# Optimization experiments

Measured on AMD Instinct MI355X. Metric: run time of the kernel, lower is better.

## Reference

```python
import jax, jax.numpy as jnp
import numpy as np

K = 2          # top-k experts
LN_EPS = 1e-5  # torch LayerNorm default


def setup_inputs() -> dict:
    key = jax.random.key(0)
    ks = jax.random.split(key, 8)
    B, D, E, H, O = 16384, 512, 16, 128, 512
    s = 0.02
    return {
        "x": jax.random.normal(ks[0], (B, D), dtype=jnp.float32),
        "gate_W": jax.random.normal(ks[1], (D, E), dtype=jnp.float32) * s,
        "gate_b": jnp.zeros((E,), dtype=jnp.float32),
        "W1": jax.random.normal(ks[2], (E, D, H), dtype=jnp.float32) * s,
        "b1": jnp.zeros((E, H), dtype=jnp.float32),
        "ln_g": jnp.ones((E, H), dtype=jnp.float32),
        "ln_b": jnp.zeros((E, H), dtype=jnp.float32),
        "W2": jax.random.normal(ks[3], (E, H, O), dtype=jnp.float32) * s,
        "b2": jnp.zeros((E, O), dtype=jnp.float32),
    }


def reference(x, gate_W, gate_b, W1, b1, ln_g, ln_b, W2, b2):
    B = x.shape[0]
    E = gate_W.shape[1]

    # gating
    gate_scores = x @ gate_W + gate_b                       # [B, E]
    topk_val, topk_idx = jax.lax.top_k(gate_scores, K)      # [B, K]

    # load-balancing aux loss
    mask = jnp.zeros((B, E), x.dtype).at[jnp.arange(B)[:, None], topk_idx].set(1.0)
    expert_usage = mask.mean(axis=0)                        # [E]
    load_balance = jnp.mean((expert_usage - 1.0 / E) ** 2)
    logp = jax.nn.log_softmax(gate_scores, axis=-1)
    entropy = (-(jnp.exp(logp) * logp).sum(axis=-1)).mean()
    aux_loss = load_balance - 0.1 * entropy

    gate_weights = jax.nn.softmax(topk_val, axis=-1)        # [B, K]

    # dense all-expert compute (as in the original torch.stack over experts)
    h = jnp.einsum('bd,edh->beh', x, W1) + b1               # [B, E, H]
    h = jax.nn.gelu(h, approximate=False)                   # torch default exact GELU
    mu = h.mean(axis=-1, keepdims=True)
    var = ((h - mu) ** 2).mean(axis=-1, keepdims=True)
    h = (h - mu) * jax.lax.rsqrt(var + LN_EPS) * ln_g + ln_b
    expert_out = jnp.einsum('beh,eho->beo', h, W2) + b2     # [B, E, O]

    # gather top-k expert outputs and combine
    sel = jnp.take_along_axis(expert_out, topk_idx[:, :, None], axis=1)  # [B, K, O]
    out = (sel * gate_weights[:, :, None]).sum(axis=1)      # [B, O]
    return out, aux_loss
```

## Files before the change

### kernel.cpp

```cpp
#include <hip/hip_runtime.h>

#define BROWS 16384
#define DDIM  512
#define NEXP  16
#define HDIM  128
#define ODIM  512
#define MAXTILES 528

typedef __attribute__((ext_vector_type(8))) short bf16x8;
typedef __attribute__((ext_vector_type(4))) float f32x4;

typedef const __attribute__((address_space(1))) unsigned GA;
typedef __attribute__((address_space(3))) unsigned LA;
#define GLD16(g, l) __builtin_amdgcn_global_load_lds((GA*)(g), (LA*)(l), 16, 0, 0)

static __device__ __forceinline__ unsigned short f2bf(float f) {
    union { float f; unsigned u; } v; v.f = f;
    unsigned r = v.u + 0x7fffu + ((v.u >> 16) & 1u);
    return (unsigned short)(r >> 16);
}
static __device__ __forceinline__ float bf2f(unsigned short h) {
    union { unsigned u; float f; } v; v.u = ((unsigned)h) << 16;
    return v.f;
}

__global__ __launch_bounds__(256)
void prep0_kernel(const float* __restrict__ gW, float* __restrict__ gwT,
                  int* __restrict__ cnt, float* __restrict__ ent_acc) {
    const int b = blockIdx.x, tid = threadIdx.x;
    if (b == 32) {
        if (tid < 16) cnt[tid] = 0;
        if (tid == 16) ent_acc[0] = 0.f;
        return;
    }
    int i = b * 256 + tid;
    int d = i >> 4, e = i & 15;
    gwT[e * 512 + d] = gW[i];
}

__global__ __launch_bounds__(256)
void gate_kernel(const float* __restrict__ x, const float* __restrict__ gwTg,
                 const float* __restrict__ gb,
                 int* cnt, float* ent_acc, int* bucket, int* topk_e, float* topk_w,
                 unsigned short* __restrict__ xb,
                 const float* __restrict__ W1, unsigned short* __restrict__ w1b,
                 const float* __restrict__ W2, unsigned short* __restrict__ w2t) {
    __shared__ __align__(16) char sbuf[33792];
    __shared__ int lcnt[16];
    __shared__ int gbase[16];
    __shared__ int entpack[32];
    __shared__ float entf;

    const int b = blockIdx.x;
    const int tid = threadIdx.x;

    if (b >= 1024) {
        if (b < 1536) {
            float (*tile)[33] = (float(*)[33])sbuf;
            int bb = b - 1024;
            int e = bb >> 5;
            int rem = bb & 31;
            int ks = rem >> 2;
            int cb = (rem & 3) * 32;
            const float* src = W1 + ((size_t)e * 512 + ks * 64) * 128 + cb;
            int c = tid & 31, r8 = tid >> 5;
            #pragma unroll
            for (int p = 0; p < 8; ++p)
                tile[p * 8 + r8][c] = src[(size_t)(p * 8 + r8) * 128 + c];
            __syncthreads();
            int k = tid & 63, c4 = tid >> 6;
            unsigned short* dst = w1b + (((size_t)e * 8 + ks) * 128 + cb) * 64;
            #pragma unroll
            for (int p = 0; p < 8; ++p)
                dst[(size_t)(c4 + p * 4) * 64 + k] = f2bf(tile[k][c4 + p * 4]);
        } else {
            float (*tile)[33] = (float(*)[33])sbuf;
            int bb = b - 1536;
            int e = bb >> 6;
            int rem = bb & 63;
            int r0 = (rem >> 4) * 32;
            int c0 = (rem & 15) * 32;
            const float* in = W2 + (size_t)e * HDIM * ODIM;
            unsigned short* out = w2t + (size_t)e * HDIM * ODIM;
            int tx = tid & 31, ty = tid >> 5;
            for (int i = ty; i < 32; i += 8)
                tile[i][tx] = in[(size_t)(r0 + i) * ODIM + c0 + tx];
            __syncthreads();
            for (int i = ty; i < 32; i += 8)
                out[(size_t)(c0 + i) * HDIM + r0 + tx] = f2bf(tile[tx][i]);
        }
        return;
    }

    float (*xs)[4][132] = (float(*)[4][132])sbuf;
    const int rb = b * 16;

    #pragma unroll
    for (int k = 0; k < 8; ++k) {
        int idx = tid + k * 256;
        int row = idx >> 7, c4 = idx & 127;
        float4 v = *reinterpret_cast<const float4*>(x + (size_t)(rb + row) * DDIM + c4 * 4);
        int dq = c4 >> 5, j = c4 & 31;
        *reinterpret_cast<float4*>(&xs[row][dq][j * 4]) = v;
        uint2 p;
        p.x = (unsigned)f2bf(v.x) | ((unsigned)f2bf(v.y) << 16);
        p.y = (unsigned)f2bf(v.z) | ((unsigned)f2bf(v.w) << 16);
        *reinterpret_cast<uint2*>(xb + (size_t)(rb + row) * DDIM + c4 * 4) = p;
    }
    if (tid < 16) lcnt[tid] = 0;
    if (tid == 0) entf = 0.f;

    const int wave = tid >> 6, lane = tid & 63;
    const int e = lane & 15, dq = lane >> 4;
    const int r0 = wave * 4;

    const float4* gw4 = reinterpret_cast<const float4*>(gwTg) + e * 128 + dq * 32;
    float gbe = gb[e];
    __syncthreads();

    float a0 = 0.f, a1 = 0.f, a2 = 0.f, a3 = 0.f;
    #pragma unroll
    for (int j = 0; j < 32; ++j) {
        float4 g  = gw4[j];
        float4 v0 = *reinterpret_cast<const float4*>(&xs[r0 + 0][dq][j * 4]);
        float4 v1 = *reinterpret_cast<const float4*>(&xs[r0 + 1][dq][j * 4]);
        float4 v2 = *reinterpret_cast<const float4*>(&xs[r0 + 2][dq][j * 4]);
        float4 v3 = *reinterpret_cast<const float4*>(&xs[r0 + 3][dq][j * 4]);
        a0 = fmaf(v0.x, g.x, a0); a0 = fmaf(v0.y, g.y, a0); a0 = fmaf(v0.z, g.z, a0); a0 = fmaf(v0.w, g.w, a0);
        a1 = fmaf(v1.x, g.x, a1); a1 = fmaf(v1.y, g.y, a1); a1 = fmaf(v1.z, g.z, a1); a1 = fmaf(v1.w, g.w, a1);
        a2 = fmaf(v2.x, g.x, a2); a2 = fmaf(v2.y, g.y, a2); a2 = fmaf(v2.z, g.z, a2); a2 = fmaf(v2.w, g.w, a2);
        a3 = fmaf(v3.x, g.x, a3); a3 = fmaf(v3.y, g.y, a3); a3 = fmaf(v3.z, g.z, a3); a3 = fmaf(v3.w, g.w, a3);
    }
    a0 += __shfl_xor(a0, 16); a0 += __shfl_xor(a0, 32);
    a1 += __shfl_xor(a1, 16); a1 += __shfl_xor(a1, 32);
    a2 += __shfl_xor(a2, 16); a2 += __shfl_xor(a2, 32);
    a3 += __shfl_xor(a3, 16); a3 += __shfl_xor(a3, 32);

    float sc = (dq == 0) ? a0 : (dq == 1) ? a1 : (dq == 2) ? a2 : a3;
    sc += gbe;

    float v0 = sc, v1 = -1e30f;
    int   i0 = e,  i1 = 255;
    #pragma unroll
    for (int k = 1; k <= 8; k <<= 1) {
        float o0 = __shfl_xor(v0, k), o1 = __shfl_xor(v1, k);
        int   oi0 = __shfl_xor(i0, k), oi1 = __shfl_xor(i1, k);
        bool gt = (o0 > v0) || (o0 == v0 && oi0 < i0);
        float n0 = gt ? o0 : v0;  int ni0 = gt ? oi0 : i0;
        float c  = gt ? v0 : o0;  int ci  = gt ? i0 : oi0;
        float d  = gt ? o1 : v1;  int di_ = gt ? oi1 : i1;
        bool g2 = (c > d) || (c == d && ci < di_);
        v0 = n0; i0 = ni0;
        v1 = g2 ? c : d;  i1 = g2 ? ci : di_;
    }

    float t = sc - v0;
    float ex = expf(t);
    float Z = ex, S1 = ex * t;
    #pragma unroll
    for (int k = 1; k <= 8; k <<= 1) {
        Z  += __shfl_xor(Z, k);
        S1 += __shfl_xor(S1, k);
    }
    float entloc = logf(Z) - S1 / Z;
    float w0 = 1.0f / (1.0f + expf(v1 - v0));

    if (e == 0) {
        int row = rb + r0 + dq;
        topk_e[row * 2]     = i0;
        topk_e[row * 2 + 1] = i1;
        topk_w[row * 2]     = w0;
        topk_w[row * 2 + 1] = 1.0f - w0;
        int ib = r0 + dq;
        int lp0 = atomicAdd(&lcnt[i0], 1);
        entpack[ib * 2]     = (row << 1) | (i0 << 15) | (lp0 << 19);
        int lp1 = atomicAdd(&lcnt[i1], 1);
        entpack[ib * 2 + 1] = ((row << 1) | 1) | (i1 << 15) | (lp1 << 19);
        atomicAdd(&entf, entloc);
    }
    __syncthreads();
    if (tid < 16) gbase[tid] = atomicAdd(&cnt[tid], lcnt[tid]);
    if (tid == 0) atomicAdd(ent_acc, entf);
    __syncthreads();
    if (tid < 32) {
        int p = entpack[tid];
        int rowslot = p & 0x7FFF;
        int ee = (p >> 15) & 15;
        int lpos = p >> 19;
        bucket[ee * BROWS + gbase[ee] + lpos] = rowslot;
    }
}

__global__ __launch_bounds__(256, 2)
void ffn_kernel(const unsigned short* __restrict__ xb,
                const unsigned short* __restrict__ w1b,
                const unsigned short* __restrict__ w2t,
                const float* __restrict__ b1, const float* __restrict__ ln_g,
                const float* __restrict__ ln_b, const float* __restrict__ topk_w,
                const int* __restrict__ cnt, const int* __restrict__ bucket,
                const float* __restrict__ ent_acc, float* __restrict__ outp,
                unsigned short* __restrict__ contrib) {
    const int b = blockIdx.x;
    const int tid = threadIdx.x;

    int e = -1, t = 0;
    {
        int o = 0;
        #pragma unroll
        for (int k = 0; k < 16; ++k) {
            int nt = (cnt[k] + 63) >> 6;
            if (b >= o && b < o + nt) { e = k; t = b - o; }
            o += nt;
        }
    }
    if (e < 0) {
        if (b == MAXTILES - 1 && tid == 0) {
            float lb = 0.f;
            for (int k = 0; k < 16; ++k) {
                float u = (float)cnt[k] * (1.f / 16384.f) - 0.0625f;
                lb += u * u;
            }
            lb *= (1.f / 16.f);
            outp[0] = lb - 0.1f * (ent_acc[0] * (1.f / 16384.f));
        }
        return;
    }
    int n = cnt[e];
    int base = t * 64;
    int rows = n - base; if (rows > 64) rows = 64;

    __shared__ __align__(16) char smem[51712];

    const int wave = tid >> 6, lane = tid & 63;
    const int l15 = lane & 15, l4 = lane >> 4;
    const int bbase = e * BROWS + base;

    if (tid < 64) {
        int idx = tid < rows ? tid : (rows - 1);
        int rs = bucket[bbase + idx];
        *(int*)(smem + 51200 + tid * 4) = rs;
        *(float*)(smem + 51456 + tid * 4) = topk_w[rs];
    }

    const int lsw = (((lane & 7) ^ ((lane >> 3) & 7)) << 4);
    int ar0 = wave * 16 + (lane >> 3);
    int ar1 = ar0 + 8;
    size_t grow0 = (size_t)(bucket[bbase + (ar0 < rows ? ar0 : rows - 1)] >> 1) * 1024;
    size_t grow1 = (size_t)(bucket[bbase + (ar1 < rows ? ar1 : rows - 1)] >> 1) * 1024;
    const char* xbp = (const char*)xb;
    const char* w1e = (const char*)w1b + (size_t)e * 131072;
    const char* w2e = (const char*)w2t + (size_t)e * 131072;
    const int sw2e = (((lane & 15) ^ (lane >> 4)) << 4);
    const int sw2o = sw2e ^ 64;

#define STAGE1(ks_, buf_) do { \
    char* ab_ = smem + (buf_) * 8192; \
    char* bb_ = smem + 16384 + (buf_) * 16384; \
    GLD16(xbp + grow0 + (ks_) * 128 + lsw, ab_ + (wave * 2 + 0) * 1024); \
    GLD16(xbp + grow1 + (ks_) * 128 + lsw, ab_ + (wave * 2 + 1) * 1024); \
    const char* s1_ = w1e + (ks_) * 16384 + ((lane >> 3) << 7) + lsw; \
    GLD16(s1_ + (wave * 4 + 0) * 1024, bb_ + (wave * 4 + 0) * 1024); \
    GLD16(s1_ + (wave * 4 + 1) * 1024, bb_ + (wave * 4 + 1) * 1024); \
    GLD16(s1_ + (wave * 4 + 2) * 1024, bb_ + (wave * 4 + 2) * 1024); \
    GLD16(s1_ + (wave * 4 + 3) * 1024, bb_ + (wave * 4 + 3) * 1024); \
} while (0)

#define STAGE2(ns_, buf_) do { \
    char* bb_ = smem + 16384 + (buf_) * 16384; \
    const char* s2_ = w2e + (size_t)(ns_) * 16384 + ((lane >> 4) << 8); \
    GLD16(s2_ + (wave * 4 + 0) * 1024 + sw2e, bb_ + (wave * 4 + 0) * 1024); \
    GLD16(s2_ + (wave * 4 + 1) * 1024 + sw2o, bb_ + (wave * 4 + 1) * 1024); \
    GLD16(s2_ + (wave * 4 + 2) * 1024 + sw2e, bb_ + (wave * 4 + 2) * 1024); \
    GLD16(s2_ + (wave * 4 + 3) * 1024 + sw2o, bb_ + (wave * 4 + 3) * 1024); \
} while (0)

    STAGE1(0, 0);
    f32x4 acc1[4][2];
    #pragma unroll
    for (int r = 0; r < 4; ++r)
        #pragma unroll
        for (int c = 0; c < 2; ++c)
            acc1[r][c] = (f32x4){0.f, 0.f, 0.f, 0.f};

    #pragma unroll
    for (int ks = 0; ks < 8; ++ks) {
        const int cur = ks & 1;
        if (ks < 7) {
            STAGE1(ks + 1, cur ^ 1);
            asm volatile("s_waitcnt vmcnt(6)" ::: "memory");
        } else {
            asm volatile("s_waitcnt vmcnt(0)" ::: "memory");
        }
        asm volatile("s_barrier" ::: "memory");
        const char* ab = smem + cur * 8192;
        const char* bb = smem + 16384 + cur * 16384;
        #pragma unroll
        for (int ks2 = 0; ks2 < 2; ++ks2) {
            const int cb = (((ks2 * 4 + l4) ^ (l15 & 7)) << 4);
            bf16x8 a[4], bg[2];
            #pragma unroll
            for (int r = 0; r < 4; ++r)
                a[r] = *(const bf16x8*)(ab + (r * 16 + l15) * 128 + cb);
            bg[0] = *(const bf16x8*)(bb + (wave * 32 + l15) * 128 + cb);
            bg[1] = *(const bf16x8*)(bb + (wave * 32 + 16 + l15) * 128 + cb);
            #pragma unroll
            for (int r = 0; r < 4; ++r) {
                acc1[r][0] = __builtin_amdgcn_mfma_f32_16x16x32_bf16(a[r], bg[0], acc1[r][0], 0, 0, 0);
                acc1[r][1] = __builtin_amdgcn_mfma_f32_16x16x32_bf16(a[r], bg[1], acc1[r][1], 0, 0, 0);
            }
        }
        asm volatile("s_waitcnt lgkmcnt(0)\n\ts_barrier" ::: "memory");
    }

    STAGE2(0, 0);

    const float* b1e = b1 + e * HDIM;
    const int c0 = wave * 32 + l15, c1 = c0 + 16;
    float bias0 = b1e[c0], bias1 = b1e[c1];
    #pragma unroll
    for (int r = 0; r < 4; ++r)
        #pragma unroll
        for (int i = 0; i < 4; ++i) {
            int row = r * 16 + l4 * 4 + i;
            float v0 = acc1[r][0][i] + bias0;
            float v1 = acc1[r][1][i] + bias1;
            v0 = 0.5f * v0 * (1.0f + erff(v0 * 0.70710678f));
            v1 = 0.5f * v1 * (1.0f + erff(v1 * 0.70710678f));
            acc1[r][0][i] = v0; acc1[r][1][i] = v1;
            float s = v0 + v1, ss = v0 * v0 + v1 * v1;
            s  += __shfl_xor(s, 1);  s  += __shfl_xor(s, 2);
            s  += __shfl_xor(s, 4);  s  += __shfl_xor(s, 8);
            ss += __shfl_xor(ss, 1); ss += __shfl_xor(ss, 2);
            ss += __shfl_xor(ss, 4); ss += __shfl_xor(ss, 8);
            if (l15 == 0) {
                *(float*)(smem + 49152 + row * 32 + wave * 8)     = s;
                *(float*)(smem + 49152 + row * 32 + wave * 8 + 4) = ss;
            }
        }
    asm volatile("s_waitcnt lgkmcnt(0)\n\ts_barrier" ::: "memory");

    {
        const float* lge = ln_g + e * HDIM;
        const float* lbe = ln_b + e * HDIM;
        float g0 = lge[c0], g1 = lge[c1], be0 = lbe[c0], be1 = lbe[c1];
        #pragma unroll
        for (int r = 0; r < 4; ++r)
            #pragma unroll
            for (int i = 0; i < 4; ++i) {
                int row = r * 16 + l4 * 4 + i;
                float4 p0 = *(const float4*)(smem + 49152 + row * 32);
                float4 p1 = *(const float4*)(smem + 49152 + row * 32 + 16);
                float s  = p0.x + p0.z + p1.x + p1.z;
                float ss = p0.y + p0.w + p1.y + p1.w;
                float mean = s * 0.0078125f;
                float var  = fmaf(-mean, mean, ss * 0.0078125f);
                float rstd = rsqrtf(var + 1e-5f);
                float w = *(const float*)(smem + 51456 + row * 4);
                float h0 = ((acc1[r][0][i] - mean) * rstd * g0 + be0) * w;
                float h1 = ((acc1[r][1][i] - mean) * rstd * g1 + be1) * w;
                int wr = (row & 7) << 4;
                *(unsigned short*)(smem + row * 256 + ((c0 * 2) ^ wr)) = f2bf(h0);
                *(unsigned short*)(smem + row * 256 + ((c1 * 2) ^ wr)) = f2bf(h1);
            }
    }
    asm volatile("s_waitcnt lgkmcnt(0)\n\ts_barrier" ::: "memory");

    bf16x8 A2[4][4];
    #pragma unroll
    for (int r = 0; r < 4; ++r)
        #pragma unroll
        for (int kk = 0; kk < 4; ++kk)
            A2[r][kk] = *(const bf16x8*)(smem + (r * 16 + l15) * 256 + ((((kk * 4 + l4) ^ (l15 & 7))) << 4));
    asm volatile("s_waitcnt lgkmcnt(0)\n\ts_barrier" ::: "memory");

    STAGE2(1, 1);
    char* patch = smem + wave * 3072;
    const int rsoff = (*(const int*)(smem + 51200 + lane * 4)) << 10;
    char* cw = (char*)contrib + rsoff + wave * 32;

    #pragma unroll
    for (int ns = 0; ns < 8; ++ns) {
        if (ns < 7) {
            asm volatile("s_waitcnt lgkmcnt(0)" ::: "memory");
            if (ns > 0) STAGE2(ns + 1, (ns + 1) & 1);
        }
        if (ns == 0)      asm volatile("s_waitcnt vmcnt(4)" ::: "memory");
        else if (ns < 7)  asm volatile("s_waitcnt vmcnt(6)" ::: "memory");
        else              asm volatile("s_waitcnt vmcnt(2)" ::: "memory");

        const char* bb = smem + 16384 + (ns & 1) * 16384;
        bf16x8 Bf[4];
        #pragma unroll
        for (int kk = 0; kk < 4; ++kk)
            Bf[kk] = *(const bf16x8*)(bb + (wave * 16 + l15) * 256 + ((((kk * 4 + l4) ^ (l15 & 7))) << 4));

        f32x4 acc2[4];
        #pragma unroll
        for (int r = 0; r < 4; ++r) acc2[r] = (f32x4){0.f, 0.f, 0.f, 0.f};
        #pragma unroll
        for (int kk = 0; kk < 4; ++kk)
            #pragma unroll
            for (int r = 0; r < 4; ++r)
                acc2[r] = __builtin_amdgcn_mfma_f32_16x16x32_bf16(A2[r][kk], Bf[kk], acc2[r], 0, 0, 0);

        #pragma unroll
        for (int r = 0; r < 4; ++r)
            #pragma unroll
            for (int i = 0; i < 4; ++i)
                *(unsigned short*)(patch + (r * 16 + l4 * 4 + i) * 48 + l15 * 2) = f2bf(acc2[r][i]);
        bf16x8 p0 = *(const bf16x8*)(patch + lane * 48);
        bf16x8 p1 = *(const bf16x8*)(patch + lane * 48 + 16);
        *(bf16x8*)(cw + ns * 128)      = p0;
        *(bf16x8*)(cw + ns * 128 + 16) = p1;
    }
#undef STAGE1
#undef STAGE2
}

__global__ __launch_bounds__(256)
void combine_kernel(const unsigned short* __restrict__ contrib, const int* __restrict__ topk_e,
                    const float* __restrict__ topk_w, const float* __restrict__ b2,
                    float* __restrict__ out) {
    int idx = blockIdx.x * 256 + threadIdx.x;
    int row = idx >> 6;
    int cb = (idx & 63) << 3;
    int e0 = topk_e[row * 2], e1 = topk_e[row * 2 + 1];
    float w0 = topk_w[row * 2], w1 = topk_w[row * 2 + 1];
    bf16x8 c0 = *reinterpret_cast<const bf16x8*>(contrib + (size_t)row * 1024 + cb);
    bf16x8 c1 = *reinterpret_cast<const bf16x8*>(contrib + (size_t)row * 1024 + 512 + cb);
    const float* b20 = b2 + e0 * ODIM + cb;
    const float* b21 = b2 + e1 * ODIM + cb;
    float res[8];
    #pragma unroll
    for (int j = 0; j < 8; ++j)
        res[j] = bf2f((unsigned short)c0[j]) + bf2f((unsigned short)c1[j]) + w0 * b20[j] + w1 * b21[j];
    float4 o0 = {res[0], res[1], res[2], res[3]};
    float4 o1 = {res[4], res[5], res[6], res[7]};
    *reinterpret_cast<float4*>(out + (size_t)row * ODIM + cb) = o0;
    *reinterpret_cast<float4*>(out + (size_t)row * ODIM + cb + 4) = o1;
}

extern "C" void kernel_launch(void* const* d_in, const int* in_sizes, int n_in,
                              void* d_out, int out_size, void* d_ws, size_t ws_size,
                              hipStream_t stream) {
    const float* x    = (const float*)d_in[0];
    const float* gW   = (const float*)d_in[1];
    const float* gb   = (const float*)d_in[2];
    const float* W1   = (const float*)d_in[3];
    const float* b1   = (const float*)d_in[4];
    const float* ln_g = (const float*)d_in[5];
    const float* ln_b = (const float*)d_in[6];
    const float* W2   = (const float*)d_in[7];
    const float* b2   = (const float*)d_in[8];
    float* out = (float*)d_out;

    char* ws = (char*)d_ws;
    int*   cnt      = (int*)(ws);
    float* ent_acc  = (float*)(ws + 64);
    int*   topk_e   = (int*)(ws + 4096);
    float* topk_w   = (float*)(ws + 135168);
    int*   bucket   = (int*)(ws + 266240);
    unsigned short* xb      = (unsigned short*)(ws + 1314816);
    unsigned short* w1b     = (unsigned short*)(ws + 18092032);
    unsigned short* w2t     = (unsigned short*)(ws + 20189184);
    unsigned short* contrib = (unsigned short*)(ws + 22286336);
    float* gwT = (float*)(ws + 22286336);

    prep0_kernel<<<33, 256, 0, stream>>>(gW, gwT, cnt, ent_acc);
    gate_kernel<<<2560, 256, 0, stream>>>(x, gwT, gb, cnt, ent_acc, bucket, topk_e, topk_w, xb,
                                          W1, w1b, W2, w2t);
    ffn_kernel<<<MAXTILES, 256, 0, stream>>>(xb, w1b, w2t, b1, ln_g, ln_b, topk_w, cnt, bucket,
                                             ent_acc, out + (out_size - 1), contrib);
    combine_kernel<<<(BROWS * ODIM / 8) / 256, 256, 0, stream>>>(contrib, topk_e, topk_w, b2, out);
}
```

Measured before the change: 86.87 us.

## Fuse top-k combine into FFN epilogue via atomic adds into zeroed output

Removes the separate combine kernel and the bf16 contrib buffer. The prep kernel now zeroes the output, and the FFN kernel adds each expert's gate-weighted result plus bias directly into the output rows with float atomicAdd. This avoids writing and re-reading the intermediate buffer. In exchange it issues one scalar atomic per output element, with scattered row addresses, and the summation order of the two experts is no longer fixed.

```diff
diff --git a/kernel.cpp b/kernel.cpp
--- a/kernel.cpp
+++ b/kernel.cpp
@@ -19,23 +19,26 @@
     unsigned r = v.u + 0x7fffu + ((v.u >> 16) & 1u);
     return (unsigned short)(r >> 16);
 }
-static __device__ __forceinline__ float bf2f(unsigned short h) {
-    union { unsigned u; float f; } v; v.u = ((unsigned)h) << 16;
-    return v.f;
-}
 
 __global__ __launch_bounds__(256)
 void prep0_kernel(const float* __restrict__ gW, float* __restrict__ gwT,
-                  int* __restrict__ cnt, float* __restrict__ ent_acc) {
+                  int* __restrict__ cnt, float* __restrict__ ent_acc,
+                  float* __restrict__ out) {
     const int b = blockIdx.x, tid = threadIdx.x;
-    if (b == 32) {
+    if (b < 32) {
+        int i = b * 256 + tid;
+        int d = i >> 4, e = i & 15;
+        gwT[e * 512 + d] = gW[i];
+    } else if (b == 32) {
         if (tid < 16) cnt[tid] = 0;
         if (tid == 16) ent_acc[0] = 0.f;
-        return;
-    }
-    int i = b * 256 + tid;
-    int d = i >> 4, e = i & 15;
-    gwT[e * 512 + d] = gW[i];
+    } else {
+        float4* o4 = reinterpret_cast<float4*>(out);
+        int i0 = (b - 33) * 256 + tid;
+        #pragma unroll
+        for (int k = 0; k < 4; ++k)
+            o4[i0 + k * 524288] = (float4){0.f, 0.f, 0.f, 0.f};
+    }
 }
 
 __global__ __launch_bounds__(256)
@@ -198,8 +201,8 @@
                 const float* __restrict__ b1, const float* __restrict__ ln_g,
                 const float* __restrict__ ln_b, const float* __restrict__ topk_w,
                 const int* __restrict__ cnt, const int* __restrict__ bucket,
-                const float* __restrict__ ent_acc, float* __restrict__ outp,
-                unsigned short* __restrict__ contrib) {
+                const float* __restrict__ ent_acc, const float* __restrict__ b2,
+                float* __restrict__ out, float* __restrict__ outp) {
     const int b = blockIdx.x;
     const int tid = threadIdx.x;
 
@@ -374,9 +377,7 @@
     asm volatile("s_waitcnt lgkmcnt(0)\n\ts_barrier" ::: "memory");
 
     STAGE2(1, 1);
-    char* patch = smem + wave * 3072;
-    const int rsoff = (*(const int*)(smem + 51200 + lane * 4)) << 10;
-    char* cw = (char*)contrib + rsoff + wave * 32;
+    const float* b2e = b2 + e * ODIM;
 
     #pragma unroll
     for (int ns = 0; ns < 8; ++ns) {
@@ -403,41 +404,22 @@
             for (int r = 0; r < 4; ++r)
                 acc2[r] = __builtin_amdgcn_mfma_f32_16x16x32_bf16(A2[r][kk], Bf[kk], acc2[r], 0, 0, 0);
 
+        const int col = ns * 64 + wave * 16 + l15;
+        const float b2v = b2e[col];
         #pragma unroll
         for (int r = 0; r < 4; ++r)
             #pragma unroll
-            for (int i = 0; i < 4; ++i)
-                *(unsigned short*)(patch + (r * 16 + l4 * 4 + i) * 48 + l15 * 2) = f2bf(acc2[r][i]);
-        bf16x8 p0 = *(const bf16x8*)(patch + lane * 48);
-        bf16x8 p1 = *(const bf16x8*)(patch + lane * 48 + 16);
-        *(bf16x8*)(cw + ns * 128)      = p0;
-        *(bf16x8*)(cw + ns * 128 + 16) = p1;
+            for (int i = 0; i < 4; ++i) {
+                int row = r * 16 + l4 * 4 + i;
+                if (row < rows) {
+                    int rs = *(const int*)(smem + 51200 + row * 4);
+                    float wv = *(const float*)(smem + 51456 + row * 4);
+                    atomicAdd(out + (size_t)(rs >> 1) * ODIM + col, acc2[r][i] + wv * b2v);
+                }
+            }
     }
 #undef STAGE1
 #undef STAGE2
-}
-
-__global__ __launch_bounds__(256)
-void combine_kernel(const unsigned short* __restrict__ contrib, const int* __restrict__ topk_e,
-                    const float* __restrict__ topk_w, const float* __restrict__ b2,
-                    float* __restrict__ out) {
-    int idx = blockIdx.x * 256 + threadIdx.x;
-    int row = idx >> 6;
-    int cb = (idx & 63) << 3;
-    int e0 = topk_e[row * 2], e1 = topk_e[row * 2 + 1];
-    float w0 = topk_w[row * 2], w1 = topk_w[row * 2 + 1];
-    bf16x8 c0 = *reinterpret_cast<const bf16x8*>(contrib + (size_t)row * 1024 + cb);
-    bf16x8 c1 = *reinterpret_cast<const bf16x8*>(contrib + (size_t)row * 1024 + 512 + cb);
-    const float* b20 = b2 + e0 * ODIM + cb;
-    const float* b21 = b2 + e1 * ODIM + cb;
-    float res[8];
-    #pragma unroll
-    for (int j = 0; j < 8; ++j)
-        res[j] = bf2f((unsigned short)c0[j]) + bf2f((unsigned short)c1[j]) + w0 * b20[j] + w1 * b21[j];
-    float4 o0 = {res[0], res[1], res[2], res[3]};
-    float4 o1 = {res[4], res[5], res[6], res[7]};
-    *reinterpret_cast<float4*>(out + (size_t)row * ODIM + cb) = o0;
-    *reinterpret_cast<float4*>(out + (size_t)row * ODIM + cb + 4) = o1;
 }
 
 extern "C" void kernel_launch(void* const* d_in, const int* in_sizes, int n_in,
@@ -460,16 +442,14 @@
     int*   topk_e   = (int*)(ws + 4096);
     float* topk_w   = (float*)(ws + 135168);
     int*   bucket   = (int*)(ws + 266240);
-    unsigned short* xb      = (unsigned short*)(ws + 1314816);
-    unsigned short* w1b     = (unsigned short*)(ws + 18092032);
-    unsigned short* w2t     = (unsigned short*)(ws + 20189184);
-    unsigned short* contrib = (unsigned short*)(ws + 22286336);
-    float* gwT = (float*)(ws + 22286336);
-
-    prep0_kernel<<<33, 256, 0, stream>>>(gW, gwT, cnt, ent_acc);
+    unsigned short* xb  = (unsigned short*)(ws + 1314816);
+    unsigned short* w1b = (unsigned short*)(ws + 18092032);
+    unsigned short* w2t = (unsigned short*)(ws + 20189184);
+    float* gwT          = (float*)(ws + 22286336);
+
+    prep0_kernel<<<2081, 256, 0, stream>>>(gW, gwT, cnt, ent_acc, out);
     gate_kernel<<<2560, 256, 0, stream>>>(x, gwT, gb, cnt, ent_acc, bucket, topk_e, topk_w, xb,
                                           W1, w1b, W2, w2t);
     ffn_kernel<<<MAXTILES, 256, 0, stream>>>(xb, w1b, w2t, b1, ln_g, ln_b, topk_w, cnt, bucket,
-                                             ent_acc, out + (out_size - 1), contrib);
-    combine_kernel<<<(BROWS * ODIM / 8) / 256, 256, 0, stream>>>(contrib, topk_e, topk_w, b2, out);
+                                             ent_acc, b2, out, out + (out_size - 1));
 }
```

Measured after the change: 119.0 us. 37.0% more time.
